# Kernel tuning notes

Measured on AMD Instinct MI355X. Metric: run time of the kernel, lower is better.

The kernel has to match this reference:

```python
import jax, jax.numpy as jnp
import numpy as np

MAX_VAL = 255.0
C1 = (0.01 * MAX_VAL) ** 2
C2 = (0.03 * MAX_VAL) ** 2


def _gauss_window(ws, sigma, channel=3):
    x = np.arange(ws, dtype=np.float64)
    g = np.exp(-((x - ws // 2) ** 2) / (2.0 * sigma ** 2))
    g = g / g.sum()
    w2 = np.outer(g, g).astype(np.float32)  # [ws, ws]
    w = np.broadcast_to(w2, (channel, 1, ws, ws)).copy()  # depthwise OIHW
    return jnp.asarray(w)


def _dwconv(x, w, pad):
    # depthwise conv2d, NCHW, groups == channels
    return jax.lax.conv_general_dilated(
        x, w, window_strides=(1, 1), padding=[(pad, pad), (pad, pad)],
        dimension_numbers=("NCHW", "OIHW", "NCHW"),
        feature_group_count=x.shape[1])


def _ssim_pair(img1, img2):
    _, c, h, w = img1.shape
    ws = min(h, w, 11)
    sigma = 1.5 * ws / 11.0
    win = _gauss_window(ws, sigma, c)
    pad = ws // 2
    mu1 = _dwconv(img1, win, pad)
    mu2 = _dwconv(img2, win, pad)
    mu1_sq, mu2_sq, mu1_mu2 = mu1 * mu1, mu2 * mu2, mu1 * mu2
    sigma1_sq = _dwconv(img1 * img1, win, pad) - mu1_sq
    sigma2_sq = _dwconv(img2 * img2, win, pad) - mu2_sq
    sigma12 = _dwconv(img1 * img2, win, pad) - mu1_mu2
    V1 = 2.0 * sigma12 + C2
    V2 = sigma1_sq + sigma2_sq + C2
    ssim_map = (2.0 * mu1_mu2 + C1) * V1 / ((mu1_sq + mu2_sq + C1) * V2)
    mcs_map = V1 / V2
    return ssim_map.mean(), mcs_map.mean()


def _avg_pool2(x):
    B, C, H, W = x.shape
    return x.reshape(B, C, H // 2, 2, W // 2, 2).mean(axis=(3, 5))


def _ms_ssim(img1, img2, levels=5):
    weight = jnp.array([0.0448, 0.2856, 0.3001, 0.2363, 0.1333], jnp.float32)
    msssim, mcs = [], []
    for _ in range(levels):
        s, m = _ssim_pair(img1, img2)
        msssim.append(s)
        mcs.append(m)
        img1 = _avg_pool2(img1)
        img2 = _avg_pool2(img2)
    msssim = jnp.stack(msssim)
    mcs = jnp.stack(mcs)
    value = jnp.prod(mcs[: levels - 1] ** weight[: levels - 1]) * msssim[levels - 1] ** weight[levels - 1]
    return 1.0 - value


def _l1_oss(img1, img2):
    _, c, h, w = img1.shape
    ws = min(h, w, 7)
    sigma = 1.1 * ws / 7.0
    win = _gauss_window(ws, sigma, c)
    return _dwconv(jnp.abs(img1 - img2), win, ws // 2).mean()


def _clr_loss(img1, img3):
    _, c, h, w = img1.shape
    ws = min(h, w, 29)
    sigma = ws / 6.0
    win = _gauss_window(ws, sigma, c)
    pad = ws // 2
    mu1 = _dwconv(img1, win, pad)
    mu3 = _dwconv(img3, win, pad)
    cw = [-0.000519, 0.07633, -0.173433, 1.435936, -1.894404, 1.556091]
    # Horner evaluation of cw[5]*x^5 + ... + cw[1]*x + cw[0]
    mu1 = ((((cw[5] * mu1 + cw[4]) * mu1 + cw[3]) * mu1 + cw[2]) * mu1 + cw[1]) * mu1 + cw[0]
    wgray = jnp.array([0.299, 0.587, 0.144], jnp.float32).reshape(1, 3, 1, 1)
    mug1 = (mu1 * wgray).sum(axis=1, keepdims=True)  # 1x1 conv over channels
    mug3 = (mu3 * wgray).sum(axis=1, keepdims=True)
    me1 = mug1.mean(axis=(2, 3), keepdims=True)
    me3 = mug3.mean(axis=(2, 3), keepdims=True)
    sc = me1 / me3
    return jnp.abs(mu1 - mu3 * sc).mean()


def setup_inputs() -> dict:
    key = jax.random.key(0)
    k1, k2, k3 = jax.random.split(key, 3)
    shape = (16, 3, 512, 512)
    return {
        "img1": jax.random.uniform(k1, shape, dtype=jnp.float32),
        "img2": jax.random.uniform(k2, shape, dtype=jnp.float32),
        "img3": jax.random.uniform(k3, shape, dtype=jnp.float32),
    }


def reference(img1, img2, img3):
    l1v = _l1_oss(img1, img2)
    clrv = _clr_loss(img1, img3)
    ssimv = _ms_ssim(img1, img2)
    return 0.4 * ssimv + 0.4 * l1v + 0.2 * clrv
```

## Files before the change

kernel.cpp:

```cpp
#include <hip/hip_runtime.h>
#include <hip/hip_fp16.h>
#include <cmath>

typedef float f2 __attribute__((ext_vector_type(2)));

struct GW7  { float g[7];  };
struct GW11 { float g[11]; };
struct GW29 { float g[29]; };

static void make_gauss(int ws, double sigma, float* out) {
    double t[32]; double s = 0.0;
    int c = ws / 2;
    for (int i = 0; i < ws; ++i) { double d = i - c; t[i] = exp(-(d * d) / (2.0 * sigma * sigma)); s += t[i]; }
    for (int i = 0; i < ws; ++i) out[i] = (float)(t[i] / s);
}

#define ACC_SLOTS 44
#define ACC_BYTES (ACC_SLOTS * 64 * sizeof(double))

__device__ __forceinline__ float poly5(float x) {
    float r = fmaf(1.556091f, x, -1.894404f);
    r = fmaf(r, x, 1.435936f);
    r = fmaf(r, x, -0.173433f);
    r = fmaf(r, x, 0.07633f);
    r = fmaf(r, x, -0.000519f);
    return r;
}

__device__ __forceinline__ float border7(int p, const GW7& gw) {
    if (p >= 3 && p <= 508) return 1.f;
    float r = 0.f;
    #pragma unroll
    for (int k = 0; k < 7; ++k) { int q = p + 3 - k; if (q >= 0 && q < 512) r += gw.g[k]; }
    return r;
}

#define SSP 49
#define SRP 33
template<bool INTER>
__global__ __launch_bounds__(256) void ssim_kernel(
    const float* __restrict__ Aim, const float* __restrict__ Bim, const f2* __restrict__ AB,
    int H, int tpp, int tilesX, GW11 gw, GW7 g7, double* __restrict__ acc, int level,
    f2* __restrict__ pooled, int Ho)
{
    constexpr int TILE = 32, IN = 42;
    __shared__ f2 lds[2 * IN * SRP];
    __shared__ float red[12];
    f2* s    = lds;
    f2* r_mu = lds;
    f2* r_sq = lds + IN * SRP;

    const int tid = threadIdx.x;
    const int bid = blockIdx.x;
    const int plane = bid / tpp;
    const int t = bid - plane * tpp;
    const int ty = t / tilesX, tx = t - ty * tilesX;
    const size_t base = (size_t)plane * H * H;
    const int oy = ty * TILE - 5, ox = tx * TILE - 5;

    for (int i = tid; i < IN * IN; i += 256) {
        int y = i / IN, x = i - y * IN;
        int gy = oy + y, gx = ox + x;
        bool ok = (gy >= 0) && (gy < H) && (gx >= 0) && (gx < H);
        size_t o = base + (size_t)gy * H + gx;
        f2 v = {0.f, 0.f};
        if (ok) {
            if (INTER) v = AB[o];
            else { v.x = Aim[o]; v.y = Bim[o]; }
        }
        s[y * SSP + x] = v;
    }
    __syncthreads();

    f2 v[18];
    const int ry = tid >> 2, rx0 = (tid & 3) * 8;
    if (tid < IN * 4) {
        #pragma unroll
        for (int l = 0; l < 18; ++l) v[l] = s[ry * SSP + rx0 + l];
    }
    if (pooled) {
        int py = tid >> 4, px = tid & 15;
        int a = (5 + 2 * py) * SSP + 5 + 2 * px;
        f2 u = s[a] + s[a + 1] + s[a + SSP] + s[a + SSP + 1];
        pooled[(size_t)plane * Ho * Ho + (size_t)(ty * 16 + py) * Ho + (tx * 16 + px)] = 0.25f * u;
    }
    float l1p = 0.f;
    if (level == 0) {
        #pragma unroll
        for (int jj = 0; jj < 4; ++jj) {
            int p = jj * 256 + tid;
            int py = p >> 5, px = p & 31;
            f2 u = s[(5 + py) * SSP + 5 + px];
            float w = border7(ty * 32 + py, g7) * border7(tx * 32 + px, g7);
            l1p += w * fabsf(u.x - u.y);
        }
    }
    __syncthreads();

    if (tid < IN * 4) {
        #pragma unroll
        for (int j = 0; j < 8; ++j) {
            f2 a = {0.f, 0.f};
            #pragma unroll
            for (int k = 0; k < 11; ++k) a = gw.g[k] * v[j + k] + a;
            r_mu[ry * SRP + rx0 + j] = a;
        }
        #pragma unroll
        for (int l = 0; l < 18; ++l) {
            f2 w;
            w.x = fmaf(v[l].x, v[l].x, v[l].y * v[l].y);
            w.y = v[l].x * v[l].y;
            v[l] = w;
        }
        #pragma unroll
        for (int j = 0; j < 8; ++j) {
            f2 a = {0.f, 0.f};
            #pragma unroll
            for (int k = 0; k < 11; ++k) a = gw.g[k] * v[j + k] + a;
            r_sq[ry * SRP + rx0 + j] = a;
        }
    }
    __syncthreads();

    const int y0 = (tid >> 5) * 4, x = tid & 31;
    float lss = 0.f, lmc = 0.f;
    {
        f2 mu[4], q[4];
        {
            f2 u[14];
            #pragma unroll
            for (int l = 0; l < 14; ++l) u[l] = r_mu[(y0 + l) * SRP + x];
            #pragma unroll
            for (int j = 0; j < 4; ++j) {
                f2 a = {0.f, 0.f};
                #pragma unroll
                for (int k = 0; k < 11; ++k) a = gw.g[k] * u[j + k] + a;
                mu[j] = a;
            }
        }
        {
            f2 u[14];
            #pragma unroll
            for (int l = 0; l < 14; ++l) u[l] = r_sq[(y0 + l) * SRP + x];
            #pragma unroll
            for (int j = 0; j < 4; ++j) {
                f2 a = {0.f, 0.f};
                #pragma unroll
                for (int k = 0; k < 11; ++k) a = gw.g[k] * u[j + k] + a;
                q[j] = a;
            }
        }
        #pragma unroll
        for (int j = 0; j < 4; ++j) {
            float m1 = mu[j].x, m2 = mu[j].y;
            float P = m1 * m2;
            float S = fmaf(m1, m1, m2 * m2);
            float V1 = 2.f * (q[j].y - P) + 58.5225f;
            float V2 = (q[j].x - S) + 58.5225f;
            float num = (2.f * P + 6.5025f) * V1;
            float SC = S + 6.5025f;
            float inv = __builtin_amdgcn_rcpf(SC * V2);
            lss = fmaf(num, inv, lss);
            lmc = fmaf(V1 * SC, inv, lmc);
        }
    }
    #pragma unroll
    for (int o = 32; o > 0; o >>= 1) {
        lss += __shfl_down(lss, o); lmc += __shfl_down(lmc, o); l1p += __shfl_down(l1p, o);
    }
    if ((tid & 63) == 0) {
        int g = tid >> 6;
        red[g * 3] = lss; red[g * 3 + 1] = lmc; red[g * 3 + 2] = l1p;
    }
    __syncthreads();
    if (tid == 0) {
        float a = red[0] + red[3] + red[6] + red[9];
        float m = red[1] + red[4] + red[7] + red[10];
        int stripe = bid & 63;
        atomicAdd(&acc[(0 + level) * 64 + stripe], (double)a);
        atomicAdd(&acc[(5 + level) * 64 + stripe], (double)m);
        if (level == 0) {
            float l1 = red[2] + red[5] + red[8] + red[11];
            atomicAdd(&acc[10 * 64 + stripe], (double)l1);
        }
    }
}

#define CRP 33
#define RING 128
template<int MODE>
__global__ __launch_bounds__(256) void clr_conv(
    const float* __restrict__ img1, const float* __restrict__ img3,
    __half2* __restrict__ pbuf, GW29 gw, double* __restrict__ acc)
{
    __shared__ f2 r[RING * CRP];
    __shared__ float red[8];
    __shared__ float sc_sh;

    const int tid = threadIdx.x, bid = blockIdx.x;
    const int plane = bid >> 4, tx = bid & 15;
    const int b = plane / 3, c = plane - b * 3;
    const float wg = (c == 0) ? 0.299f : (c == 1 ? 0.587f : 0.144f);
    const size_t base = (size_t)plane * (512 * 512);

    if (MODE == 2 && tid < 64) {
        double m1 = acc[(12 + b) * 64 + tid];
        double m3 = acc[(28 + b) * 64 + tid];
        #pragma unroll
        for (int o = 32; o > 0; o >>= 1) { m1 += __shfl_down(m1, o); m3 += __shfl_down(m3, o); }
        if (tid == 0) sc_sh = (float)(m1 / m3);
    }

    const int rrow = tid >> 2, xq = tid & 3;
    const int c0 = tx * 8 + xq * 2 - 4;

    auto rowconv = [&](int lr) {
        const int ri = ((lr + RING) & (RING - 1)) * CRP + xq * 8;
        if (lr < 0 || lr >= 512) {
            #pragma unroll
            for (int j = 0; j < 8; ++j) r[ri + j] = (f2){0.f, 0.f};
            return;
        }
        const float4* row1 = (const float4*)(img1 + base + (size_t)lr * 512);
        const float4* row3 = (const float4*)(img3 + base + (size_t)lr * 512);
        float w[40];
        float o1[8];
        #pragma unroll
        for (int k = 0; k < 10; ++k) {
            int cc = c0 + k;
            float4 f = {0.f, 0.f, 0.f, 0.f};
            if (cc >= 0 && cc < 128) f = row1[cc];
            w[4 * k] = f.x; w[4 * k + 1] = f.y; w[4 * k + 2] = f.z; w[4 * k + 3] = f.w;
        }
        #pragma unroll
        for (int j = 0; j < 8; ++j) {
            float a = 0.f;
            #pragma unroll
            for (int k = 0; k < 29; ++k) a = fmaf(gw.g[k], w[2 + j + k], a);
            o1[j] = a;
        }
        #pragma unroll
        for (int k = 0; k < 10; ++k) {
            int cc = c0 + k;
            float4 f = {0.f, 0.f, 0.f, 0.f};
            if (cc >= 0 && cc < 128) f = row3[cc];
            w[4 * k] = f.x; w[4 * k + 1] = f.y; w[4 * k + 2] = f.z; w[4 * k + 3] = f.w;
        }
        #pragma unroll
        for (int j = 0; j < 8; ++j) {
            float a = 0.f;
            #pragma unroll
            for (int k = 0; k < 29; ++k) a = fmaf(gw.g[k], w[2 + j + k], a);
            r[ri + j] = (f2){o1[j], a};
        }
    };

    rowconv(-14 + rrow);
    __syncthreads();

    float p1 = 0.f, p3 = 0.f;
    const int x = tid & 31;
    #pragma unroll 1
    for (int ck = 0; ck < 8; ++ck) {
        {
            int lr = 50 + 64 * ck + rrow;
            if (lr <= 525) rowconv(lr);
        }
        __syncthreads();
        #pragma unroll
        for (int g = 0; g < 2; ++g) {
            const int y0 = 64 * ck + g * 32 + (tid >> 5) * 4;
            f2 u[32];
            #pragma unroll
            for (int l = 0; l < 32; ++l)
                u[l] = r[(((y0 - 14 + l) + RING) & (RING - 1)) * CRP + x];
            #pragma unroll
            for (int j = 0; j < 4; ++j) {
                f2 a = {0.f, 0.f};
                #pragma unroll
                for (int k = 0; k < 29; ++k) a = gw.g[k] * u[j + k] + a;
                float p = poly5(a.x);
                if (MODE == 2) {
                    p1 += fabsf(p - a.y * sc_sh);
                } else {
                    p1 += p; p3 += a.y;
                    if (MODE == 0)
                        pbuf[base + (size_t)(y0 + j) * 512 + (tx * 32 + x)] =
                            __floats2half2_rn(p, a.y);
                }
            }
        }
        if (ck < 7) __syncthreads();
    }

    if (MODE != 2) { p1 *= wg; p3 *= wg; }
    #pragma unroll
    for (int o = 32; o > 0; o >>= 1) { p1 += __shfl_down(p1, o); p3 += __shfl_down(p3, o); }
    if ((tid & 63) == 0) { red[(tid >> 6) * 2] = p1; red[(tid >> 6) * 2 + 1] = p3; }
    __syncthreads();
    if (tid == 0) {
        float a1 = red[0] + red[2] + red[4] + red[6];
        int stripe = bid & 63;
        if (MODE == 2) {
            atomicAdd(&acc[11 * 64 + stripe], (double)a1);
        } else {
            float a3 = red[1] + red[3] + red[5] + red[7];
            atomicAdd(&acc[(12 + b) * 64 + stripe], (double)a1);
            atomicAdd(&acc[(28 + b) * 64 + stripe], (double)a3);
        }
    }
}

__global__ __launch_bounds__(256) void clr_fin(
    const __half2* __restrict__ pbuf, double* __restrict__ acc)
{
    __shared__ float red[4];
    __shared__ float sc_sh;
    const int tid = threadIdx.x, bid = blockIdx.x;
    const int b = bid / 192, sub = bid - b * 192;
    if (tid < 64) {
        double m1 = acc[(12 + b) * 64 + tid];
        double m3 = acc[(28 + b) * 64 + tid];
        #pragma unroll
        for (int o = 32; o > 0; o >>= 1) { m1 += __shfl_down(m1, o); m3 += __shfl_down(m3, o); }
        if (tid == 0) sc_sh = (float)(m1 / m3);
    }
    __syncthreads();
    const float sc = sc_sh;
    const size_t bo = (size_t)b * 786432 + (size_t)sub * 4096;
    float s = 0.f;
    #pragma unroll
    for (int it = 0; it < 8; ++it) {
        size_t i = bo + it * 512 + tid * 2;
        float2 a = __half22float2(pbuf[i]);
        float2 c = __half22float2(pbuf[i + 1]);
        s += fabsf(a.x - a.y * sc) + fabsf(c.x - c.y * sc);
    }
    #pragma unroll
    for (int o = 32; o > 0; o >>= 1) s += __shfl_down(s, o);
    if ((tid & 63) == 0) red[tid >> 6] = s;
    __syncthreads();
    if (tid == 0)
        atomicAdd(&acc[11 * 64 + (bid & 63)], (double)(red[0] + red[1] + red[2] + red[3]));
}

__global__ void finalize_kernel(const double* __restrict__ acc, float* __restrict__ out)
{
    __shared__ double sums[ACC_SLOTS];
    int t = threadIdx.x;
    if (t < ACC_SLOTS) {
        double s = 0.0;
        for (int i = 0; i < 64; ++i) s += acc[t * 64 + i];
        sums[t] = s;
    }
    __syncthreads();
    if (t == 0) {
        const double w[5] = {0.0448, 0.2856, 0.3001, 0.2363, 0.1333};
        double value = 1.0;
        for (int l = 0; l < 5; ++l) {
            double dim = (double)(512 >> l);
            double cnt = 48.0 * dim * dim;
            double mval = (l < 4) ? (sums[5 + l] / cnt) : (sums[l] / cnt);
            value *= pow(mval, w[l]);
        }
        double n0 = 48.0 * 512.0 * 512.0;
        double l1v = sums[10] / n0;
        double clrv = sums[11] / n0;
        out[0] = (float)(0.4 * (1.0 - value) + 0.4 * l1v + 0.2 * clrv);
    }
}

extern "C" void kernel_launch(void* const* d_in, const int* in_sizes, int n_in,
                              void* d_out, int out_size, void* d_ws, size_t ws_size,
                              hipStream_t stream)
{
    (void)in_sizes; (void)n_in; (void)out_size;
    const float* img1 = (const float*)d_in[0];
    const float* img2 = (const float*)d_in[1];
    const float* img3 = (const float*)d_in[2];
    float* out = (float*)d_out;
    double* acc = (double*)d_ws;

    GW11 g11; make_gauss(11, 1.5, g11.g);
    GW7  g7;  make_gauss(7, 1.1, g7.g);
    GW29 g29; make_gauss(29, 29.0 / 6.0, g29.g);

    hipMemsetAsync(d_ws, 0, ACC_BYTES, stream);

    f2* pyr = (f2*)((char*)d_ws + 32768);
    size_t offs[4];
    offs[0] = 0;
    offs[1] = offs[0] + (size_t)48 * 256 * 256;
    offs[2] = offs[1] + (size_t)48 * 128 * 128;
    offs[3] = offs[2] + (size_t)48 * 64 * 64;
    const size_t PYRF2 = offs[3] + (size_t)48 * 32 * 32;

    const f2* cur = nullptr;
    int H = 512;
    for (int l = 0; l < 5; ++l) {
        int tilesX = H / 32; int tpp = tilesX * tilesX;
        f2* pooled = (l < 4) ? (pyr + offs[l]) : nullptr;
        int Ho = H / 2;
        if (l == 0)
            ssim_kernel<false><<<48 * tpp, 256, 0, stream>>>(
                img1, img2, nullptr, H, tpp, tilesX, g11, g7, acc, l, pooled, Ho);
        else
            ssim_kernel<true><<<48 * tpp, 256, 0, stream>>>(
                nullptr, nullptr, cur, H, tpp, tilesX, g11, g7, acc, l, pooled, Ho);
        cur = pooled; H = Ho;
    }

    const size_t poff = 32768 + PYRF2 * sizeof(f2);
    const size_t PBYTES = (size_t)48 * 512 * 512 * sizeof(__half2);
    __half2* pbuf = (__half2*)((char*)d_ws + poff);
    if (ws_size >= poff + PBYTES) {
        clr_conv<0><<<768, 256, 0, stream>>>(img1, img3, pbuf, g29, acc);
        clr_fin<<<3072, 256, 0, stream>>>(pbuf, acc);
    } else {
        clr_conv<1><<<768, 256, 0, stream>>>(img1, img3, pbuf, g29, acc);
        clr_conv<2><<<768, 256, 0, stream>>>(img1, img3, pbuf, g29, acc);
    }

    finalize_kernel<<<1, 64, 0, stream>>>(acc, out);
}
```

Measured before the change: 223.4 us.

## Fuse level-0 SSIM and CLR conv into one heterogeneous kernel launch

Adds a fused_l0 kernel whose first 3072 blocks run the 29-tap CLR separable convolution and whose remaining blocks run the level-0 SSIM/L1 tile work. The CLR part moves from 768 blocks that each own a full column strip to 3072 blocks of 128-row chunks, with the horizontal pass staged in an fp16 ring buffer. The point is to raise parallelism and let the large CLR pass overlap with level-0 SSIM in a single launch. The cost is extra halo recomputation per row chunk and extra fp16 rounding of the intermediate horizontal results.

New measurement: 224.9 us. Within noise of the previous version (+0.7%).

```diff
diff --git a/kernel.cpp b/kernel.cpp
--- a/kernel.cpp
+++ b/kernel.cpp
@@ -37,6 +37,9 @@
 
 #define SSP 49
 #define SRP 33
+#define CRP 33
+#define RING 128
+
 template<bool INTER>
 __global__ __launch_bounds__(256) void ssim_kernel(
     const float* __restrict__ Aim, const float* __restrict__ Bim, const f2* __restrict__ AB,
@@ -186,8 +189,253 @@
     }
 }
 
-#define CRP 33
-#define RING 128
+__global__ __launch_bounds__(256) void fused_l0(
+    const float* __restrict__ img1, const float* __restrict__ img2,
+    const float* __restrict__ img3,
+    GW11 g11, GW7 g7, GW29 g29,
+    __half2* __restrict__ pbuf, f2* __restrict__ pooled, double* __restrict__ acc)
+{
+    constexpr int IN = 42;
+    __shared__ f2 lds[2 * IN * SRP];
+    __shared__ float red[12];
+
+    const int tid = threadIdx.x;
+    const int bid = blockIdx.x;
+
+    if (bid < 3072) {
+        __half2* ring = (__half2*)lds;
+        const int plane = bid >> 6, rr = bid & 63;
+        const int tx = rr >> 2, q = rr & 3;
+        const int base_row = q * 128;
+        const int b = plane / 3, c = plane - b * 3;
+        const float wg = (c == 0) ? 0.299f : (c == 1 ? 0.587f : 0.144f);
+        const size_t base = (size_t)plane * (512 * 512);
+
+        const int rrow = tid >> 2, xq = tid & 3;
+        const int c0 = tx * 8 + xq * 2 - 4;
+
+        auto rowconv = [&](int rel) {
+            const int slot = (rel + RING) & (RING - 1);
+            __half2* rr2 = ring + slot * CRP + xq * 8;
+            const int lr = base_row + rel;
+            if (lr < 0 || lr >= 512) {
+                #pragma unroll
+                for (int j = 0; j < 8; ++j) rr2[j] = __floats2half2_rn(0.f, 0.f);
+                return;
+            }
+            const float4* row1 = (const float4*)(img1 + base + (size_t)lr * 512);
+            const float4* row3 = (const float4*)(img3 + base + (size_t)lr * 512);
+            float w[40];
+            float o1[8];
+            #pragma unroll
+            for (int k = 0; k < 10; ++k) {
+                int cc = c0 + k;
+                float4 f = {0.f, 0.f, 0.f, 0.f};
+                if (cc >= 0 && cc < 128) f = row1[cc];
+                w[4 * k] = f.x; w[4 * k + 1] = f.y; w[4 * k + 2] = f.z; w[4 * k + 3] = f.w;
+            }
+            #pragma unroll
+            for (int j = 0; j < 8; ++j) {
+                float a = 0.f;
+                #pragma unroll
+                for (int k = 0; k < 29; ++k) a = fmaf(g29.g[k], w[2 + j + k], a);
+                o1[j] = a;
+            }
+            #pragma unroll
+            for (int k = 0; k < 10; ++k) {
+                int cc = c0 + k;
+                float4 f = {0.f, 0.f, 0.f, 0.f};
+                if (cc >= 0 && cc < 128) f = row3[cc];
+                w[4 * k] = f.x; w[4 * k + 1] = f.y; w[4 * k + 2] = f.z; w[4 * k + 3] = f.w;
+            }
+            #pragma unroll
+            for (int j = 0; j < 8; ++j) {
+                float a = 0.f;
+                #pragma unroll
+                for (int k = 0; k < 29; ++k) a = fmaf(g29.g[k], w[2 + j + k], a);
+                rr2[j] = __floats2half2_rn(o1[j], a);
+            }
+        };
+
+        rowconv(-14 + rrow);
+        __syncthreads();
+
+        float p1 = 0.f, p3 = 0.f;
+        const int x = tid & 31;
+        for (int ck = 0; ck < 2; ++ck) {
+            int rel = 50 + 64 * ck + rrow;
+            if (rel <= 141) rowconv(rel);
+            __syncthreads();
+            #pragma unroll
+            for (int g = 0; g < 2; ++g) {
+                const int y0 = 64 * ck + g * 32 + (tid >> 5) * 4;
+                f2 u[32];
+                #pragma unroll
+                for (int l = 0; l < 32; ++l) {
+                    float2 tf = __half22float2(ring[(((y0 - 14 + l) + RING) & (RING - 1)) * CRP + x]);
+                    u[l] = (f2){tf.x, tf.y};
+                }
+                #pragma unroll
+                for (int j = 0; j < 4; ++j) {
+                    f2 a = {0.f, 0.f};
+                    #pragma unroll
+                    for (int k = 0; k < 29; ++k) a = g29.g[k] * u[j + k] + a;
+                    float p = poly5(a.x);
+                    p1 += p; p3 += a.y;
+                    pbuf[base + (size_t)(base_row + y0 + j) * 512 + (tx * 32 + x)] =
+                        __floats2half2_rn(p, a.y);
+                }
+            }
+            if (ck == 0) __syncthreads();
+        }
+
+        p1 *= wg; p3 *= wg;
+        #pragma unroll
+        for (int o = 32; o > 0; o >>= 1) { p1 += __shfl_down(p1, o); p3 += __shfl_down(p3, o); }
+        if ((tid & 63) == 0) { red[(tid >> 6) * 2] = p1; red[(tid >> 6) * 2 + 1] = p3; }
+        __syncthreads();
+        if (tid == 0) {
+            float a1 = red[0] + red[2] + red[4] + red[6];
+            float a3 = red[1] + red[3] + red[5] + red[7];
+            int stripe = bid & 63;
+            atomicAdd(&acc[(12 + b) * 64 + stripe], (double)a1);
+            atomicAdd(&acc[(28 + b) * 64 + stripe], (double)a3);
+        }
+        return;
+    }
+
+    f2* s    = lds;
+    f2* r_mu = lds;
+    f2* r_sq = lds + IN * SRP;
+
+    const int sbid = bid - 3072;
+    const int plane = sbid >> 8;
+    const int t = sbid & 255;
+    const int ty = t >> 4, tx = t & 15;
+    const size_t base = (size_t)plane * (512 * 512);
+    const int oy = ty * 32 - 5, ox = tx * 32 - 5;
+
+    for (int i = tid; i < IN * IN; i += 256) {
+        int y = i / IN, x = i - y * IN;
+        int gy = oy + y, gx = ox + x;
+        bool ok = (gy >= 0) && (gy < 512) && (gx >= 0) && (gx < 512);
+        size_t o = base + (size_t)gy * 512 + gx;
+        f2 v = {0.f, 0.f};
+        if (ok) { v.x = img1[o]; v.y = img2[o]; }
+        s[y * SSP + x] = v;
+    }
+    __syncthreads();
+
+    f2 v[18];
+    const int ry = tid >> 2, rx0 = (tid & 3) * 8;
+    if (tid < IN * 4) {
+        #pragma unroll
+        for (int l = 0; l < 18; ++l) v[l] = s[ry * SSP + rx0 + l];
+    }
+    {
+        int py = tid >> 4, px = tid & 15;
+        int a = (5 + 2 * py) * SSP + 5 + 2 * px;
+        f2 u = s[a] + s[a + 1] + s[a + SSP] + s[a + SSP + 1];
+        pooled[(size_t)plane * 256 * 256 + (size_t)(ty * 16 + py) * 256 + (tx * 16 + px)] = 0.25f * u;
+    }
+    float l1p = 0.f;
+    #pragma unroll
+    for (int jj = 0; jj < 4; ++jj) {
+        int p = jj * 256 + tid;
+        int py = p >> 5, px = p & 31;
+        f2 u = s[(5 + py) * SSP + 5 + px];
+        float w = border7(ty * 32 + py, g7) * border7(tx * 32 + px, g7);
+        l1p += w * fabsf(u.x - u.y);
+    }
+    __syncthreads();
+
+    if (tid < IN * 4) {
+        #pragma unroll
+        for (int j = 0; j < 8; ++j) {
+            f2 a = {0.f, 0.f};
+            #pragma unroll
+            for (int k = 0; k < 11; ++k) a = g11.g[k] * v[j + k] + a;
+            r_mu[ry * SRP + rx0 + j] = a;
+        }
+        #pragma unroll
+        for (int l = 0; l < 18; ++l) {
+            f2 w;
+            w.x = fmaf(v[l].x, v[l].x, v[l].y * v[l].y);
+            w.y = v[l].x * v[l].y;
+            v[l] = w;
+        }
+        #pragma unroll
+        for (int j = 0; j < 8; ++j) {
+            f2 a = {0.f, 0.f};
+            #pragma unroll
+            for (int k = 0; k < 11; ++k) a = g11.g[k] * v[j + k] + a;
+            r_sq[ry * SRP + rx0 + j] = a;
+        }
+    }
+    __syncthreads();
+
+    const int y0 = (tid >> 5) * 4, x = tid & 31;
+    float lss = 0.f, lmc = 0.f;
+    {
+        f2 mu[4], q[4];
+        {
+            f2 u[14];
+            #pragma unroll
+            for (int l = 0; l < 14; ++l) u[l] = r_mu[(y0 + l) * SRP + x];
+            #pragma unroll
+            for (int j = 0; j < 4; ++j) {
+                f2 a = {0.f, 0.f};
+                #pragma unroll
+                for (int k = 0; k < 11; ++k) a = g11.g[k] * u[j + k] + a;
+                mu[j] = a;
+            }
+        }
+        {
+            f2 u[14];
+            #pragma unroll
+            for (int l = 0; l < 14; ++l) u[l] = r_sq[(y0 + l) * SRP + x];
+            #pragma unroll
+            for (int j = 0; j < 4; ++j) {
+                f2 a = {0.f, 0.f};
+                #pragma unroll
+                for (int k = 0; k < 11; ++k) a = g11.g[k] * u[j + k] + a;
+                q[j] = a;
+            }
+        }
+        #pragma unroll
+        for (int j = 0; j < 4; ++j) {
+            float m1 = mu[j].x, m2 = mu[j].y;
+            float P = m1 * m2;
+            float S = fmaf(m1, m1, m2 * m2);
+            float V1 = 2.f * (q[j].y - P) + 58.5225f;
+            float V2 = (q[j].x - S) + 58.5225f;
+            float num = (2.f * P + 6.5025f) * V1;
+            float SC = S + 6.5025f;
+            float inv = __builtin_amdgcn_rcpf(SC * V2);
+            lss = fmaf(num, inv, lss);
+            lmc = fmaf(V1 * SC, inv, lmc);
+        }
+    }
+    #pragma unroll
+    for (int o = 32; o > 0; o >>= 1) {
+        lss += __shfl_down(lss, o); lmc += __shfl_down(lmc, o); l1p += __shfl_down(l1p, o);
+    }
+    if ((tid & 63) == 0) {
+        int g = tid >> 6;
+        red[g * 3] = lss; red[g * 3 + 1] = lmc; red[g * 3 + 2] = l1p;
+    }
+    __syncthreads();
+    if (tid == 0) {
+        float a = red[0] + red[3] + red[6] + red[9];
+        float m = red[1] + red[4] + red[7] + red[10];
+        int stripe = bid & 63;
+        atomicAdd(&acc[0 * 64 + stripe], (double)a);
+        atomicAdd(&acc[5 * 64 + stripe], (double)m);
+        float l1 = red[2] + red[5] + red[8] + red[11];
+        atomicAdd(&acc[10 * 64 + stripe], (double)l1);
+    }
+}
+
 template<int MODE>
 __global__ __launch_bounds__(256) void clr_conv(
     const float* __restrict__ img1, const float* __restrict__ img3,
@@ -284,9 +532,6 @@
                     p1 += fabsf(p - a.y * sc_sh);
                 } else {
                     p1 += p; p3 += a.y;
-                    if (MODE == 0)
-                        pbuf[base + (size_t)(y0 + j) * 512 + (tx * 32 + x)] =
-                            __floats2half2_rn(p, a.y);
                 }
             }
         }
@@ -395,29 +640,34 @@
     offs[3] = offs[2] + (size_t)48 * 64 * 64;
     const size_t PYRF2 = offs[3] + (size_t)48 * 32 * 32;
 
-    const f2* cur = nullptr;
-    int H = 512;
-    for (int l = 0; l < 5; ++l) {
+    const size_t poff = 32768 + PYRF2 * sizeof(f2);
+    const size_t PBYTES = (size_t)48 * 512 * 512 * sizeof(__half2);
+    __half2* pbuf = (__half2*)((char*)d_ws + poff);
+    const bool bigws = (ws_size >= poff + PBYTES);
+
+    if (bigws) {
+        fused_l0<<<15360, 256, 0, stream>>>(img1, img2, img3, g11, g7, g29,
+                                            pbuf, pyr + offs[0], acc);
+    } else {
+        ssim_kernel<false><<<12288, 256, 0, stream>>>(
+            img1, img2, nullptr, 512, 256, 16, g11, g7, acc, 0, pyr + offs[0], 256);
+        clr_conv<1><<<768, 256, 0, stream>>>(img1, img3, pbuf, g29, acc);
+    }
+
+    const f2* cur = pyr + offs[0];
+    int H = 256;
+    for (int l = 1; l < 5; ++l) {
         int tilesX = H / 32; int tpp = tilesX * tilesX;
         f2* pooled = (l < 4) ? (pyr + offs[l]) : nullptr;
         int Ho = H / 2;
-        if (l == 0)
-            ssim_kernel<false><<<48 * tpp, 256, 0, stream>>>(
-                img1, img2, nullptr, H, tpp, tilesX, g11, g7, acc, l, pooled, Ho);
-        else
-            ssim_kernel<true><<<48 * tpp, 256, 0, stream>>>(
-                nullptr, nullptr, cur, H, tpp, tilesX, g11, g7, acc, l, pooled, Ho);
+        ssim_kernel<true><<<48 * tpp, 256, 0, stream>>>(
+            nullptr, nullptr, cur, H, tpp, tilesX, g11, g7, acc, l, pooled, Ho);
         cur = pooled; H = Ho;
     }
 
-    const size_t poff = 32768 + PYRF2 * sizeof(f2);
-    const size_t PBYTES = (size_t)48 * 512 * 512 * sizeof(__half2);
-    __half2* pbuf = (__half2*)((char*)d_ws + poff);
-    if (ws_size >= poff + PBYTES) {
-        clr_conv<0><<<768, 256, 0, stream>>>(img1, img3, pbuf, g29, acc);
+    if (bigws) {
         clr_fin<<<3072, 256, 0, stream>>>(pbuf, acc);
     } else {
-        clr_conv<1><<<768, 256, 0, stream>>>(img1, img3, pbuf, g29, acc);
         clr_conv<2><<<768, 256, 0, stream>>>(img1, img3, pbuf, g29, acc);
     }
 
```
